# Kernel tuning notes

Measured on AMD Instinct MI355X. Metric: run time of the kernel, lower is better.

Reference implementation:

```python
import jax, jax.numpy as jnp
import numpy as np

B, T, F_IN, F_OUT, N, TP, K = 32, 12, 16, 32, 2048, 12, 3
RED = 4  # SE reduction ratio


def _conv2d(x, w, b):
    # x: [b,c,h,w_] NCHW, w: [o,i,kh,kw] OIHW, VALID padding (matches nn.Conv2d default)
    y = jax.lax.conv_general_dilated(x, w, window_strides=(1, 1), padding='VALID',
                                     dimension_numbers=('NCHW', 'OIHW', 'NCHW'))
    return y + b[None, :, None, None]


def _tconv(x, w, b, tp):
    # Tconv1: conv (1,2) -> self-pad time axis back to tp with trailing slices -> relu
    y = _conv2d(x, w, b)
    t = y.shape[-1]
    if t < tp:
        y = jnp.concatenate([y[..., -(tp - t):], y], axis=-1)
    return jax.nn.relu(y)


def setup_inputs() -> dict:
    rng = np.random.default_rng(0)
    # symmetric nonneg adjacency
    W = rng.random((N, N), dtype=np.float32)
    W = (W + W.T) * 0.5
    D = np.diag(W.sum(axis=1))
    L = (D - W).astype(np.float32)
    # lambda_max via power iteration (replaces scipy eigs 'LR')
    v = rng.standard_normal(N).astype(np.float32)
    for _ in range(100):
        v = L @ v
        v /= np.linalg.norm(v)
    lam = float(v @ (L @ v))
    Lt = (2.0 * L / lam - np.eye(N, dtype=np.float32)).astype(np.float32)
    # NOTE: original code uses ELEMENTWISE '*' (numpy) in the Chebyshev recurrence; replicate faithfully
    cheb = [np.eye(N, dtype=np.float32), Lt.copy()]
    for _ in range(2, K):
        cheb.append(2.0 * Lt * cheb[-1] - cheb[-2])
    cheb = jnp.asarray(np.stack(cheb))  # [K, N, N]

    key = jax.random.key(0)
    ks = jax.random.split(key, 16)
    s = 0.05
    hid = T // RED
    return {
        'x': jax.random.normal(ks[0], (B, T, F_IN, N), dtype=jnp.float32),
        'cheb': cheb,
        'theta1': jax.random.normal(ks[1], (K, F_IN, F_OUT), dtype=jnp.float32) * s,
        'theta2': jax.random.normal(ks[2], (K, F_OUT, F_OUT), dtype=jnp.float32) * s,
        'mlp1_w': jax.random.normal(ks[3], (hid, T), dtype=jnp.float32) * s,
        'mlp1_b': jnp.zeros((hid,), dtype=jnp.float32),
        'mlp2_w': jax.random.normal(ks[4], (T, hid), dtype=jnp.float32) * s,
        'mlp2_b': jnp.zeros((T,), dtype=jnp.float32),
        'tc1_w': jax.random.normal(ks[5], (F_OUT, F_OUT, 1, 2), dtype=jnp.float32) * s,
        'tc1_b': jnp.zeros((F_OUT,), dtype=jnp.float32),
        'tc2_w': jax.random.normal(ks[6], (F_OUT, F_OUT, 1, 2), dtype=jnp.float32) * s,
        'tc2_b': jnp.zeros((F_OUT,), dtype=jnp.float32),
        'res_w': jax.random.normal(ks[7], (F_OUT, F_IN, 1, 1), dtype=jnp.float32) * s,
        'res_b': jnp.zeros((F_OUT,), dtype=jnp.float32),
        'ln_g': jnp.ones((N,), dtype=jnp.float32),
        'ln_b': jnp.zeros((N,), dtype=jnp.float32),
    }


def reference(x, cheb, theta1, theta2, mlp1_w, mlp1_b, mlp2_w, mlp2_b,
              tc1_w, tc1_b, tc2_w, tc2_b, res_w, res_b, ln_g, ln_b):
    # --- SE channel attention over the t axis ---
    att = x.mean(axis=(2, 3))                            # [b,t] (AvgPool over full (f,n))
    att = jax.nn.relu(att @ mlp1_w.T + mlp1_b)
    att = jax.nn.sigmoid(att @ mlp2_w.T + mlp2_b)
    x_att = x * att[:, :, None, None]                    # [b,t,f,n]

    # --- Chebyshev graph conv: fused over time t and order k ---
    def gconv(h, theta):
        # original: for t, for k: (h[b,:,f,t] @ T_k) then (@ theta_k), summed over k
        z = jnp.einsum('btfm,kmn->bktfn', h, cheb)       # graph mixing, [b,K,t,f,n]
        return jnp.einsum('bktfn,kfo->bton', z, theta)   # feature mixing + k-sum -> [b,t,o,n]

    xg = jax.nn.relu(gconv(x_att, theta1))
    xg = jax.nn.relu(gconv(xg, theta2))                  # [b,t,F_OUT,n]

    # --- temporal convs ---
    xt = _tconv(xg.transpose(0, 2, 3, 1), tc1_w, tc1_b, TP)   # [b,F_OUT,n,TP]
    xt = _tconv(xt, tc2_w, tc2_b, TP).transpose(0, 3, 1, 2)   # [b,TP,F_OUT,n]

    # --- residual 1x1 conv on the original input ---
    tshort = xg.shape[1] - xt.shape[1]                   # == 0 with t == tp
    x_res = _conv2d(x[:, tshort:].transpose(0, 2, 3, 1), res_w, res_b).transpose(0, 3, 1, 2)

    y = xt + x_res                                       # [b,TP,F_OUT,n]
    # LayerNorm over last (node) axis, eps=1e-5, biased variance (torch default)
    mu = y.mean(axis=-1, keepdims=True)
    var = ((y - mu) ** 2).mean(axis=-1, keepdims=True)
    y = (y - mu) / jnp.sqrt(var + 1e-5) * ln_g + ln_b
    return jax.nn.relu(y)
```

## Files before the change

kernel.cpp:

```cpp
#include <hip/hip_runtime.h>

#define DI __device__ __forceinline__

typedef __attribute__((ext_vector_type(8))) short short8;
typedef __attribute__((ext_vector_type(4))) float f32x4;

static constexpr int Bb  = 32;
static constexpr int Tt  = 12;
static constexpr int FIN = 16;
static constexpr int NN  = 2048;
static constexpr int HID = 3;
static constexpr int M1  = Bb*Tt*FIN;
static constexpr int M2  = Bb*Tt*32;

DI float b2f(unsigned short u){
  unsigned int v = ((unsigned int)u) << 16;
  float f; __builtin_memcpy(&f, &v, 4); return f;
}
DI unsigned short f2b(float f){
  unsigned int v; __builtin_memcpy(&v, &f, 4);
  v = v + 0x7FFFu + ((v >> 16) & 1u);
  return (unsigned short)(v >> 16);
}
DI float ld(const void* p, size_t i, int flag){
  return flag ? b2f(((const unsigned short*)p)[i]) : ((const float*)p)[i];
}

typedef __attribute__((address_space(1))) const unsigned int g_u32;
typedef __attribute__((address_space(3))) unsigned int l_u32;
DI void gll16(const unsigned short* g, unsigned short* l){
  __builtin_amdgcn_global_load_lds((g_u32*)g, (l_u32*)l, 16, 0, 0);
}

__global__ void k_sniff(const unsigned short* __restrict__ x, int* __restrict__ flag){
  int tid = threadIdx.x;
  float v = b2f(x[tid*2]);
  int bad = (!(v == v)) || (fabsf(v) > 1e6f);
  unsigned long long m = __ballot(bad);
  if (tid == 0) *flag = (m == 0ull) ? 1 : 0;
}

__global__ void k_convert(const void* __restrict__ src, unsigned short* __restrict__ dst,
                          long long n8, const int* __restrict__ flagp, long long off){
  int flag = *flagp;
  long long i = (long long)blockIdx.x*256 + threadIdx.x;
  if (i >= n8) return;
  size_t base = (size_t)i * 8;
  if (flag){
    *(uint4*)(dst + base) = *(const uint4*)((const unsigned short*)src + off + base);
  } else {
    const float* f = (const float*)src + off + base;
    unsigned short o[8];
    #pragma unroll
    for (int j = 0; j < 8; ++j) o[j] = f2b(f[j]);
    uint4 ov; __builtin_memcpy(&ov, o, 16);
    *(uint4*)(dst + base) = ov;
  }
}

__global__ void k_att_mean(const void* __restrict__ x, float* __restrict__ att0,
                           const int* __restrict__ flagp){
  int flag = *flagp;
  int bt = blockIdx.x; int tid = threadIdx.x;
  size_t base = (size_t)bt * FIN * NN;
  float s = 0.f;
  for (int i = tid; i < FIN*NN; i += 256) s += ld(x, base + i, flag);
  for (int off = 32; off; off >>= 1) s += __shfl_down(s, off);
  __shared__ float red[4];
  if ((tid & 63) == 0) red[tid >> 6] = s;
  __syncthreads();
  if (tid == 0) att0[bt] = (red[0]+red[1]+red[2]+red[3]) * (1.f / (FIN*NN));
}

__global__ void k_att_mlp(const float* __restrict__ att0,
                          const void* __restrict__ m1w, const void* __restrict__ m1b,
                          const void* __restrict__ m2w, const void* __restrict__ m2b,
                          float* __restrict__ att, const int* __restrict__ flagp){
  int flag = *flagp;
  int b = threadIdx.x;
  if (b >= Bb) return;
  float a[Tt];
  #pragma unroll
  for (int t = 0; t < Tt; ++t) a[t] = att0[b*Tt + t];
  float h[HID];
  #pragma unroll
  for (int j = 0; j < HID; ++j){
    float s = ld(m1b, j, flag);
    #pragma unroll
    for (int t = 0; t < Tt; ++t) s += a[t] * ld(m1w, j*Tt + t, flag);
    h[j] = s > 0.f ? s : 0.f;
  }
  #pragma unroll
  for (int t = 0; t < Tt; ++t){
    float s = ld(m2b, t, flag);
    #pragma unroll
    for (int j = 0; j < HID; ++j) s += h[j] * ld(m2w, t*HID + j, flag);
    att[b*Tt + t] = 1.f / (1.f + expf(-s));
  }
}

DI void stage_tile(const unsigned short* __restrict__ Ag,
                   const unsigned short* __restrict__ chb,
                   unsigned short* Ad, unsigned short* Bd,
                   int row0, int gn0, int kk0, int tid){
  #pragma unroll
  for (int p = 0; p < 2; ++p){
    int s = tid + p*256, r = s >> 2, j = s & 3;
    gll16(Ag + (size_t)(row0 + r)*NN + kk0 + ((j ^ (r & 3)) << 3), Ad + (s << 3));
  }
  #pragma unroll
  for (int p = 0; p < 4; ++p){
    int s = tid + p*256, k = s >> 9, rem = s & 511, r = rem >> 2, j = rem & 3;
    gll16(chb + (size_t)k*NN*NN + (size_t)(gn0 + r)*NN + kk0 + ((j ^ (r & 3)) << 3), Bd + (s << 3));
  }
}

DI void compute_tile(const unsigned short* As, const unsigned short* Bs,
                     f32x4 (&acc)[2][8][2], int w, int cc, int q){
  short8 af[8];
  #pragma unroll
  for (int mt = 0; mt < 8; ++mt)
    af[mt] = *(const short8*)(As + ((mt*16 + cc) << 5) + ((q ^ (cc & 3)) << 3));
  #pragma unroll
  for (int k = 0; k < 2; ++k){
    #pragma unroll
    for (int ns = 0; ns < 2; ++ns){
      int r = w*32 + ns*16 + cc;
      short8 bv = *(const short8*)(Bs + (((k << 7) + r) << 5) + ((q ^ (cc & 3)) << 3));
      #pragma unroll
      for (int mt = 0; mt < 8; ++mt)
        acc[k][mt][ns] = __builtin_amdgcn_mfma_f32_16x16x32_bf16(af[mt], bv, acc[k][mt][ns], 0, 0, 0);
    }
  }
}

template <int SCALE, int F>
__global__ __launch_bounds__(256, 2)
void k_gemm(const unsigned short* __restrict__ Ag,
            const float* __restrict__ att,
            const unsigned short* __restrict__ chb,
            const void* __restrict__ theta,
            unsigned short* __restrict__ X,
            const int* __restrict__ flagp){
  constexpr int Kp = (F == 16) ? 64 : 96;
  constexpr int PP = (F == 16) ? 72 : 104;
  constexpr int G  = 128 / F;
  constexpr int NKB = Kp / 32;
  constexpr int BUF = 128*32 + 2*128*32;

  __shared__ __align__(16) unsigned short SMEM[2*BUF];
  __shared__ __align__(16) unsigned short TT[32*PP];

  int flag = *flagp;
  int tid  = threadIdx.x;
  int w    = tid >> 6, lane = tid & 63, q = lane >> 4, cc = lane & 15;
  int row0 = blockIdx.x * 128;
  int gn0  = blockIdx.y * 128;

  for (int idx = tid; idx < 32*PP; idx += 256){
    int o = idx / PP, kk = idx % PP;
    float v = (kk < 3*F) ? ld(theta, (size_t)kk*32 + o, flag) : 0.f;
    TT[idx] = f2b(v);
  }

  unsigned short* A0 = SMEM;
  unsigned short* B0 = SMEM + 4096;
  unsigned short* A1 = SMEM + BUF;
  unsigned short* B1 = SMEM + BUF + 4096;

  f32x4 zero4 = {0.f, 0.f, 0.f, 0.f};
  f32x4 acc[2][8][2];
  #pragma unroll
  for (int k = 0; k < 2; ++k)
    #pragma unroll
    for (int mt = 0; mt < 8; ++mt)
      #pragma unroll
      for (int ns = 0; ns < 2; ++ns) acc[k][mt][ns] = zero4;

  stage_tile(Ag, chb, A0, B0, row0, gn0, 0, tid);
  __syncthreads();

  for (int it = 0; it < 62; it += 2){
    stage_tile(Ag, chb, A1, B1, row0, gn0, (it+1)*32, tid);
    compute_tile(A0, B0, acc, w, cc, q);
    __syncthreads();
    stage_tile(Ag, chb, A0, B0, row0, gn0, (it+2)*32, tid);
    compute_tile(A1, B1, acc, w, cc, q);
    __syncthreads();
  }
  stage_tile(Ag, chb, A1, B1, row0, gn0, 63*32, tid);
  compute_tile(A0, B0, acc, w, cc, q);
  __syncthreads();
  compute_tile(A1, B1, acc, w, cc, q);
  __syncthreads();

  unsigned short* zs = SMEM + w * (32*PP);

  short8 afm[2][NKB];
  #pragma unroll
  for (int mt_o = 0; mt_o < 2; ++mt_o)
    #pragma unroll
    for (int kb = 0; kb < NKB; ++kb)
      afm[mt_o][kb] = *(const short8*)(TT + (mt_o*16 + cc)*PP + kb*32 + q*8);

  if (F == 16){
    if (lane < 32){
      #pragma unroll
      for (int j = 0; j < 4; ++j) *(uint2*)(zs + lane*PP + 48 + j*4) = make_uint2(0u, 0u);
    }
  }

  int bt0 = row0 / F;
  #pragma unroll
  for (int g = 0; g < G; ++g){
    float sc = SCALE ? att[bt0 + g] : 1.f;
    #pragma unroll
    for (int pass = 0; pass < F/16; ++pass){
      int rf = pass*16 + (lane >> 2), c8 = (lane & 3) * 8;
      uint4 u = *(const uint4*)(Ag + (size_t)(row0 + g*F + rf)*NN + gn0 + w*32 + c8);
      unsigned short sp[8]; __builtin_memcpy(sp, &u, 16);
      #pragma unroll
      for (int e = 0; e < 8; ++e){
        unsigned short val = SCALE ? f2b(b2f(sp[e]) * sc) : sp[e];
        zs[(c8 + e)*PP + rf] = val;
      }
    }
    #pragma unroll
    for (int k = 0; k < 2; ++k)
      #pragma unroll
      for (int mt_l = 0; mt_l < F/16; ++mt_l)
        #pragma unroll
        for (int ns = 0; ns < 2; ++ns){
          int mt = g*(F/16) + mt_l;
          f32x4 v = acc[k][mt][ns];
          #pragma unroll
          for (int r = 0; r < 4; ++r){
            float pv = SCALE ? v[r] * sc : v[r];
            zs[(ns*16 + cc)*PP + F*(k+1) + mt_l*16 + q*4 + r] = f2b(pv);
          }
        }
    #pragma unroll
    for (int mt_o = 0; mt_o < 2; ++mt_o)
      #pragma unroll
      for (int ch = 0; ch < 2; ++ch){
        f32x4 am = zero4;
        #pragma unroll
        for (int kb = 0; kb < NKB; ++kb){
          short8 bm = *(const short8*)(zs + (ch*16 + cc)*PP + kb*32 + q*8);
          am = __builtin_amdgcn_mfma_f32_16x16x32_bf16(afm[mt_o][kb], bm, am, 0, 0, 0);
        }
        #pragma unroll
        for (int r = 0; r < 4; ++r){
          int o = mt_o*16 + q*4 + r;
          float v = am[r]; v = v > 0.f ? v : 0.f;
          X[((size_t)((bt0 + g)*32 + o))*NN + gn0 + w*32 + ch*16 + cc] = f2b(v);
        }
      }
  }
}

__global__ void k_tconv1(const unsigned short* __restrict__ xin,
                         const void* __restrict__ wgt, const void* __restrict__ bias,
                         unsigned short* __restrict__ yout, const int* __restrict__ flagp){
  int flag = *flagp;
  __shared__ float wl[32*32*2];
  __shared__ float bl[32];
  int tid = threadIdx.x;
  for (int i = tid; i < 2048; i += 256) wl[i] = ld(wgt, i, flag);
  if (tid < 32) bl[tid] = ld(bias, tid, flag);
  __syncthreads();
  int bt = blockIdx.x, b = bt / 12, t = bt % 12;
  int c = (t == 0) ? 10 : (t - 1);
  int n = blockIdx.y*256 + tid;
  const unsigned short* p0 = xin + ((size_t)(b*12 + c  )*32)*NN + n;
  const unsigned short* p1 = xin + ((size_t)(b*12 + c+1)*32)*NN + n;
  float acc[32];
  #pragma unroll
  for (int o = 0; o < 32; ++o) acc[o] = bl[o];
  for (int i = 0; i < 32; ++i){
    float v0 = b2f(p0[(size_t)i*NN]);
    float v1 = b2f(p1[(size_t)i*NN]);
    #pragma unroll
    for (int o = 0; o < 32; ++o) acc[o] += v0*wl[o*64 + i*2] + v1*wl[o*64 + i*2 + 1];
  }
  unsigned short* op = yout + ((size_t)bt*32)*NN + n;
  #pragma unroll
  for (int o = 0; o < 32; ++o){ float v = acc[o]; op[(size_t)o*NN] = f2b(v > 0.f ? v : 0.f); }
}

__global__ __launch_bounds__(256, 2)
void k_tail(const unsigned short* __restrict__ yp,
            const void* __restrict__ x,
            const void* __restrict__ w2, const void* __restrict__ b2v,
            const void* __restrict__ rw, const void* __restrict__ rbv,
            const void* __restrict__ lng, const void* __restrict__ lnb,
            void* __restrict__ out, const int* __restrict__ flagp){
  int flag = *flagp;
  __shared__ float wt0[32*16], wt1[32*16];
  __shared__ float rt[16*16];
  __shared__ float bcv[16], rbc[16];
  __shared__ float redS[4*16], redS2[4*16];
  int tid = threadIdx.x;
  int bt = blockIdx.x, og = blockIdx.y, o0 = og*16;
  int b = bt / 12, t = bt % 12, c = (t == 0) ? 10 : (t - 1);
  for (int idx = tid; idx < 512; idx += 256){
    int i = idx >> 4, oo = idx & 15;
    wt0[idx] = ld(w2, (size_t)(o0 + oo)*64 + i*2,     flag);
    wt1[idx] = ld(w2, (size_t)(o0 + oo)*64 + i*2 + 1, flag);
  }
  if (tid < 256){
    int i = tid >> 4, oo = tid & 15;
    rt[tid] = ld(rw, (size_t)(o0 + oo)*16 + i, flag);
  }
  if (tid < 16){ bcv[tid] = ld(b2v, o0 + tid, flag); rbc[tid] = ld(rbv, o0 + tid, flag); }
  __syncthreads();
  float acc[16][8];
  #pragma unroll
  for (int oo = 0; oo < 16; ++oo)
    #pragma unroll
    for (int nn = 0; nn < 8; ++nn) acc[oo][nn] = bcv[oo];
  const unsigned short* p0 = yp + ((size_t)(b*12 + c  )*32)*NN;
  const unsigned short* p1 = yp + ((size_t)(b*12 + c+1)*32)*NN;
  for (int i = 0; i < 32; ++i){
    float v0[8], v1[8];
    #pragma unroll
    for (int nn = 0; nn < 8; ++nn){
      int n = nn*256 + tid;
      v0[nn] = b2f(p0[(size_t)i*NN + n]);
      v1[nn] = b2f(p1[(size_t)i*NN + n]);
    }
    #pragma unroll
    for (int oo = 0; oo < 16; ++oo){
      float w0 = wt0[i*16 + oo];
      float w1 = wt1[i*16 + oo];
      #pragma unroll
      for (int nn = 0; nn < 8; ++nn) acc[oo][nn] += v0[nn]*w0 + v1[nn]*w1;
    }
  }
  #pragma unroll
  for (int oo = 0; oo < 16; ++oo)
    #pragma unroll
    for (int nn = 0; nn < 8; ++nn){ float v = acc[oo][nn]; acc[oo][nn] = (v > 0.f ? v : 0.f) + rbc[oo]; }
  size_t xbase = ((size_t)(b*12 + t)*16)*NN;
  for (int i = 0; i < 16; ++i){
    float xv[8];
    #pragma unroll
    for (int nn = 0; nn < 8; ++nn) xv[nn] = ld(x, xbase + (size_t)i*NN + nn*256 + tid, flag);
    #pragma unroll
    for (int oo = 0; oo < 16; ++oo){
      float r = rt[i*16 + oo];
      #pragma unroll
      for (int nn = 0; nn < 8; ++nn) acc[oo][nn] += xv[nn]*r;
    }
  }
  int lane = tid & 63, wv = tid >> 6;
  #pragma unroll
  for (int oo = 0; oo < 16; ++oo){
    float s = 0.f, s2 = 0.f;
    #pragma unroll
    for (int nn = 0; nn < 8; ++nn){ float v = acc[oo][nn]; s += v; s2 += v*v; }
    for (int off = 32; off; off >>= 1){ s += __shfl_down(s, off); s2 += __shfl_down(s2, off); }
    if (lane == 0){ redS[wv*16 + oo] = s; redS2[wv*16 + oo] = s2; }
  }
  __syncthreads();
  size_t obase = ((size_t)((b*12 + t)*32 + o0))*NN;
  #pragma unroll
  for (int nn = 0; nn < 8; ++nn){
    int n = nn*256 + tid;
    float g = ld(lng, n, flag), be = ld(lnb, n, flag);
    #pragma unroll
    for (int oo = 0; oo < 16; ++oo){
      float S  = redS [oo] + redS [16 + oo] + redS [32 + oo] + redS [48 + oo];
      float S2 = redS2[oo] + redS2[16 + oo] + redS2[32 + oo] + redS2[48 + oo];
      float m = S * (1.f/2048.f);
      float var = S2 * (1.f/2048.f) - m*m;
      float inv = rsqrtf(var + 1e-5f);
      float v = (acc[oo][nn] - m)*inv*g + be;
      v = v > 0.f ? v : 0.f;
      if (flag) ((unsigned short*)out)[obase + (size_t)oo*NN + n] = f2b(v);
      else      ((float*)out)[obase + (size_t)oo*NN + n] = v;
    }
  }
}

extern "C" void kernel_launch(void* const* d_in, const int* in_sizes, int n_in,
                              void* d_out, int out_size, void* d_ws, size_t ws_size,
                              hipStream_t stream){
  const void* x    = d_in[0];
  const void* cheb = d_in[1];
  const void* th1  = d_in[2];
  const void* th2  = d_in[3];
  const void* m1w  = d_in[4];
  const void* m1b  = d_in[5];
  const void* m2w  = d_in[6];
  const void* m2b  = d_in[7];
  const void* t1w  = d_in[8];
  const void* t1b  = d_in[9];
  const void* t2w  = d_in[10];
  const void* t2b  = d_in[11];
  const void* rw   = d_in[12];
  const void* rb   = d_in[13];
  const void* lng  = d_in[14];
  const void* lnb  = d_in[15];
  char* ws = (char*)d_ws;

  int*   flag  = (int*)ws;
  float* att0  = (float*)(ws + 4096);
  float* att   = (float*)(ws + 8192);
  unsigned short* xb  = (unsigned short*)(ws + 16384);
  unsigned short* chb = xb + (size_t)M1*NN;
  unsigned short* X1  = chb + (size_t)2*NN*NN;
  unsigned short* X2  = (unsigned short*)d_out;
  unsigned short* Y1  = X1;

  k_sniff  <<<1, 64, 0, stream>>>((const unsigned short*)x, flag);
  k_convert<<<((long long)M1*NN/8 + 255)/256, 256, 0, stream>>>(x, xb, (long long)M1*NN/8, flag, 0);
  k_convert<<<((long long)2*NN*NN/8 + 255)/256, 256, 0, stream>>>(cheb, chb, (long long)2*NN*NN/8, flag, (long long)NN*NN);
  k_att_mean<<<384, 256, 0, stream>>>(x, att0, flag);
  k_att_mlp <<<1, 64, 0, stream>>>(att0, m1w, m1b, m2w, m2b, att, flag);

  k_gemm<1,16><<<dim3(M1/128, 16), 256, 0, stream>>>(xb, att, chb, th1, X1, flag);
  k_gemm<0,32><<<dim3(M2/128, 16), 256, 0, stream>>>(X1, att, chb, th2, X2, flag);

  k_tconv1<<<dim3(384, 8), 256, 0, stream>>>(X2, t1w, t1b, Y1, flag);
  k_tail  <<<dim3(384, 2), 256, 0, stream>>>(Y1, x, t2w, t2b, rw, rb, lng, lnb, d_out, flag);
}
```

Before: 772.9 us.

## Triple-buffer GEMM staging with vmcnt waits and fuse attention mean into convert

```diff
diff --git a/kernel.cpp b/kernel.cpp
--- a/kernel.cpp
+++ b/kernel.cpp
@@ -32,8 +32,10 @@
   __builtin_amdgcn_global_load_lds((g_u32*)g, (l_u32*)l, 16, 0, 0);
 }
 
-__global__ void k_sniff(const unsigned short* __restrict__ x, int* __restrict__ flag){
+__global__ void k_sniff(const unsigned short* __restrict__ x, int* __restrict__ flag,
+                        float* __restrict__ att0){
   int tid = threadIdx.x;
+  for (int j = tid; j < Bb*Tt; j += 64) att0[j] = 0.f;
   float v = b2f(x[tid*2]);
   int bad = (!(v == v)) || (fabsf(v) > 1e6f);
   unsigned long long m = __ballot(bad);
@@ -41,35 +43,41 @@
 }
 
 __global__ void k_convert(const void* __restrict__ src, unsigned short* __restrict__ dst,
-                          long long n8, const int* __restrict__ flagp, long long off){
+                          long long n8, const int* __restrict__ flagp, long long off,
+                          float* __restrict__ att0){
   int flag = *flagp;
-  long long i = (long long)blockIdx.x*256 + threadIdx.x;
-  if (i >= n8) return;
-  size_t base = (size_t)i * 8;
-  if (flag){
-    *(uint4*)(dst + base) = *(const uint4*)((const unsigned short*)src + off + base);
-  } else {
-    const float* f = (const float*)src + off + base;
-    unsigned short o[8];
-    #pragma unroll
-    for (int j = 0; j < 8; ++j) o[j] = f2b(f[j]);
-    uint4 ov; __builtin_memcpy(&ov, o, 16);
-    *(uint4*)(dst + base) = ov;
-  }
-}
-
-__global__ void k_att_mean(const void* __restrict__ x, float* __restrict__ att0,
-                           const int* __restrict__ flagp){
-  int flag = *flagp;
-  int bt = blockIdx.x; int tid = threadIdx.x;
-  size_t base = (size_t)bt * FIN * NN;
+  int tid = threadIdx.x;
+  long long i = (long long)blockIdx.x*256 + tid;
   float s = 0.f;
-  for (int i = tid; i < FIN*NN; i += 256) s += ld(x, base + i, flag);
-  for (int off = 32; off; off >>= 1) s += __shfl_down(s, off);
-  __shared__ float red[4];
-  if ((tid & 63) == 0) red[tid >> 6] = s;
-  __syncthreads();
-  if (tid == 0) att0[bt] = (red[0]+red[1]+red[2]+red[3]) * (1.f / (FIN*NN));
+  if (i < n8){
+    size_t base = (size_t)i * 8;
+    if (flag){
+      uint4 u = *(const uint4*)((const unsigned short*)src + off + base);
+      *(uint4*)(dst + base) = u;
+      if (att0){
+        unsigned short sp[8]; __builtin_memcpy(sp, &u, 16);
+        #pragma unroll
+        for (int j = 0; j < 8; ++j) s += b2f(sp[j]);
+      }
+    } else {
+      const float* f = (const float*)src + off + base;
+      unsigned short o[8];
+      #pragma unroll
+      for (int j = 0; j < 8; ++j){ float fv = f[j]; o[j] = f2b(fv); s += fv; }
+      uint4 ov; __builtin_memcpy(&ov, o, 16);
+      *(uint4*)(dst + base) = ov;
+    }
+  }
+  if (att0){
+    for (int o2 = 32; o2; o2 >>= 1) s += __shfl_down(s, o2);
+    __shared__ float red[4];
+    if ((tid & 63) == 0) red[tid >> 6] = s;
+    __syncthreads();
+    if (tid == 0){
+      int bt = (int)(blockIdx.x >> 4);
+      atomicAdd(&att0[bt], red[0] + red[1] + red[2] + red[3]);
+    }
+  }
 }
 
 __global__ void k_att_mlp(const float* __restrict__ att0,
@@ -81,7 +89,7 @@
   if (b >= Bb) return;
   float a[Tt];
   #pragma unroll
-  for (int t = 0; t < Tt; ++t) a[t] = att0[b*Tt + t];
+  for (int t = 0; t < Tt; ++t) a[t] = att0[b*Tt + t] * (1.f / (FIN*NN));
   float h[HID];
   #pragma unroll
   for (int j = 0; j < HID; ++j){
@@ -132,6 +140,17 @@
         acc[k][mt][ns] = __builtin_amdgcn_mfma_f32_16x16x32_bf16(af[mt], bv, acc[k][mt][ns], 0, 0, 0);
     }
   }
+}
+
+DI void wait_bar_6(){
+  asm volatile("s_waitcnt vmcnt(6)" ::: "memory");
+  __builtin_amdgcn_s_barrier();
+  asm volatile("" ::: "memory");
+}
+DI void wait_bar_0(){
+  asm volatile("s_waitcnt vmcnt(0)" ::: "memory");
+  __builtin_amdgcn_s_barrier();
+  asm volatile("" ::: "memory");
 }
 
 template <int SCALE, int F>
@@ -148,7 +167,7 @@
   constexpr int NKB = Kp / 32;
   constexpr int BUF = 128*32 + 2*128*32;
 
-  __shared__ __align__(16) unsigned short SMEM[2*BUF];
+  __shared__ __align__(16) unsigned short SMEM[3*BUF];
   __shared__ __align__(16) unsigned short TT[32*PP];
 
   int flag = *flagp;
@@ -163,11 +182,6 @@
     TT[idx] = f2b(v);
   }
 
-  unsigned short* A0 = SMEM;
-  unsigned short* B0 = SMEM + 4096;
-  unsigned short* A1 = SMEM + BUF;
-  unsigned short* B1 = SMEM + BUF + 4096;
-
   f32x4 zero4 = {0.f, 0.f, 0.f, 0.f};
   f32x4 acc[2][8][2];
   #pragma unroll
@@ -177,21 +191,23 @@
       #pragma unroll
       for (int ns = 0; ns < 2; ++ns) acc[k][mt][ns] = zero4;
 
-  stage_tile(Ag, chb, A0, B0, row0, gn0, 0, tid);
-  __syncthreads();
-
-  for (int it = 0; it < 62; it += 2){
-    stage_tile(Ag, chb, A1, B1, row0, gn0, (it+1)*32, tid);
-    compute_tile(A0, B0, acc, w, cc, q);
-    __syncthreads();
-    stage_tile(Ag, chb, A0, B0, row0, gn0, (it+2)*32, tid);
-    compute_tile(A1, B1, acc, w, cc, q);
-    __syncthreads();
-  }
-  stage_tile(Ag, chb, A1, B1, row0, gn0, 63*32, tid);
-  compute_tile(A0, B0, acc, w, cc, q);
-  __syncthreads();
-  compute_tile(A1, B1, acc, w, cc, q);
+  unsigned short *Ac = SMEM,           *Bc = SMEM + 4096;
+  unsigned short *An = SMEM +   BUF,   *Bn = SMEM +   BUF + 4096;
+  unsigned short *Af = SMEM + 2*BUF,   *Bf = SMEM + 2*BUF + 4096;
+
+  stage_tile(Ag, chb, Ac, Bc, row0, gn0, 0,  tid);
+  stage_tile(Ag, chb, An, Bn, row0, gn0, 32, tid);
+
+  for (int it = 0; it < 63; ++it){
+    wait_bar_6();
+    if (it < 62) stage_tile(Ag, chb, Af, Bf, row0, gn0, (it + 2) * 32, tid);
+    compute_tile(Ac, Bc, acc, w, cc, q);
+    unsigned short* tA = Ac; Ac = An; An = Af; Af = tA;
+    unsigned short* tB = Bc; Bc = Bn; Bn = Bf; Bf = tB;
+  }
+  wait_bar_0();
+  compute_tile(Ac, Bc, acc, w, cc, q);
+
   __syncthreads();
 
   unsigned short* zs = SMEM + w * (32*PP);
@@ -413,10 +429,9 @@
   unsigned short* X2  = (unsigned short*)d_out;
   unsigned short* Y1  = X1;
 
-  k_sniff  <<<1, 64, 0, stream>>>((const unsigned short*)x, flag);
-  k_convert<<<((long long)M1*NN/8 + 255)/256, 256, 0, stream>>>(x, xb, (long long)M1*NN/8, flag, 0);
-  k_convert<<<((long long)2*NN*NN/8 + 255)/256, 256, 0, stream>>>(cheb, chb, (long long)2*NN*NN/8, flag, (long long)NN*NN);
-  k_att_mean<<<384, 256, 0, stream>>>(x, att0, flag);
+  k_sniff  <<<1, 64, 0, stream>>>((const unsigned short*)x, flag, att0);
+  k_convert<<<((long long)M1*NN/8 + 255)/256, 256, 0, stream>>>(x, xb, (long long)M1*NN/8, flag, 0, att0);
+  k_convert<<<((long long)2*NN*NN/8 + 255)/256, 256, 0, stream>>>(cheb, chb, (long long)2*NN*NN/8, flag, (long long)NN*NN, nullptr);
   k_att_mlp <<<1, 64, 0, stream>>>(att0, m1w, m1b, m2w, m2b, att, flag);
 
   k_gemm<1,16><<<dim3(M1/128, 16), 256, 0, stream>>>(xb, att, chb, th1, X1, flag);
```

New measurement: 778.5 us. Within noise of the previous version (+0.7%).
